# Optimization experiments

Measured on AMD Instinct MI355X. Metric: run time of the kernel, lower is better.

## Reference

```python
import jax, jax.numpy as jnp
import numpy as np


def setup_inputs() -> dict:
    key = jax.random.key(0)
    tensor = jax.random.normal(key, (1024, 32768), dtype=jnp.float32)
    return {"tensor": tensor}


def reference(tensor):
    # Fused equivalent of the per-channel Python loop: for each channel
    # (leading dim), compute min and max over all remaining elements.
    C = tensor.shape[0]
    flat = tensor.reshape(C, -1)  # [C, N]
    min_vals = jnp.min(flat, axis=1)  # [C]
    max_vals = jnp.max(flat, axis=1)  # [C]
    return min_vals, max_vals
```

## Files before the change

kernel.cpp:

```cpp
#include <hip/hip_runtime.h>
#include <math.h>


__global__ __launch_bounds__(256) void cw_minmax_kernel(
    const float* __restrict__ in, float* __restrict__ out, int nvec, int C) {
    const int c = blockIdx.x;
    const float4* __restrict__ row =
        reinterpret_cast<const float4*>(in) + (size_t)c * nvec;

    float vmin = INFINITY;
    float vmax = -INFINITY;

    for (int i = threadIdx.x; i < nvec; i += blockDim.x) {
        float4 v = row[i];
        vmin = fminf(vmin, fminf(fminf(v.x, v.y), fminf(v.z, v.w)));
        vmax = fmaxf(vmax, fmaxf(fmaxf(v.x, v.y), fmaxf(v.z, v.w)));
    }

    #pragma unroll
    for (int off = 32; off > 0; off >>= 1) {
        vmin = fminf(vmin, __shfl_down(vmin, off, 64));
        vmax = fmaxf(vmax, __shfl_down(vmax, off, 64));
    }

    __shared__ float smin[4];
    __shared__ float smax[4];
    const int wave = threadIdx.x >> 6;
    const int lane = threadIdx.x & 63;
    if (lane == 0) { smin[wave] = vmin; smax[wave] = vmax; }
    __syncthreads();

    if (threadIdx.x == 0) {
        float m = smin[0], M = smax[0];
        #pragma unroll
        for (int w = 1; w < 4; ++w) {
            m = fminf(m, smin[w]);
            M = fmaxf(M, smax[w]);
        }
        out[c] = m;
        out[C + c] = M;
    }
}

extern "C" void kernel_launch(void* const* d_in, const int* in_sizes, int n_in,
                              void* d_out, int out_size, void* d_ws, size_t ws_size,
                              hipStream_t stream) {
    const float* in = (const float*)d_in[0];
    float* out = (float*)d_out;

    const int C = out_size / 2;
    const int N = in_sizes[0] / C;
    const int nvec = N / 4;

    cw_minmax_kernel<<<C, 256, 0, stream>>>(in, out, nvec, C);
}
```

Measured before the change: 186.7 us.

## Use 1024-thread blocks with fully unrolled register-batched row loads

Replaces the strided loop with a templated kernel where each of 1024 threads issues all its float4 loads up front (8 per thread for N=32768), then reduces them. The aim is to raise memory-level parallelism and cut loop overhead so the bandwidth-bound scan keeps more loads in flight. A scalar generic fallback handles shapes that do not fit. The cost is higher register pressure and a larger cross-wave reduction of 16 waves per block.

Result: no change. 184.0 us (-1.5%).

```diff
diff --git a/kernel.cpp b/kernel.cpp
--- a/kernel.cpp
+++ b/kernel.cpp
@@ -2,29 +2,35 @@
 #include <math.h>
 
 
-__global__ __launch_bounds__(256) void cw_minmax_kernel(
+#define BS 1024
+
+template <int PER>
+__global__ __launch_bounds__(BS) void cw_minmax_spec(
     const float* __restrict__ in, float* __restrict__ out, int nvec, int C) {
     const int c = blockIdx.x;
     const float4* __restrict__ row =
         reinterpret_cast<const float4*>(in) + (size_t)c * nvec;
 
-    float vmin = INFINITY;
-    float vmax = -INFINITY;
+    float4 v[PER];
+    #pragma unroll
+    for (int k = 0; k < PER; ++k)
+        v[k] = row[threadIdx.x + k * BS];
 
-    for (int i = threadIdx.x; i < nvec; i += blockDim.x) {
-        float4 v = row[i];
-        vmin = fminf(vmin, fminf(fminf(v.x, v.y), fminf(v.z, v.w)));
-        vmax = fmaxf(vmax, fmaxf(fmaxf(v.x, v.y), fmaxf(v.z, v.w)));
+    float vmin = INFINITY, vmax = -INFINITY;
+    #pragma unroll
+    for (int k = 0; k < PER; ++k) {
+        vmin = fminf(vmin, fminf(fminf(v[k].x, v[k].y), fminf(v[k].z, v[k].w)));
+        vmax = fmaxf(vmax, fmaxf(fmaxf(v[k].x, v[k].y), fmaxf(v[k].z, v[k].w)));
     }
 
     #pragma unroll
     for (int off = 32; off > 0; off >>= 1) {
-        vmin = fminf(vmin, __shfl_down(vmin, off, 64));
-        vmax = fmaxf(vmax, __shfl_down(vmax, off, 64));
+        vmin = fminf(vmin, __shfl_xor(vmin, off, 64));
+        vmax = fmaxf(vmax, __shfl_xor(vmax, off, 64));
     }
 
-    __shared__ float smin[4];
-    __shared__ float smax[4];
+    __shared__ float smin[BS / 64];
+    __shared__ float smax[BS / 64];
     const int wave = threadIdx.x >> 6;
     const int lane = threadIdx.x & 63;
     if (lane == 0) { smin[wave] = vmin; smax[wave] = vmax; }
@@ -33,6 +39,39 @@
     if (threadIdx.x == 0) {
         float m = smin[0], M = smax[0];
         #pragma unroll
+        for (int w = 1; w < BS / 64; ++w) {
+            m = fminf(m, smin[w]);
+            M = fmaxf(M, smax[w]);
+        }
+        out[c] = m;
+        out[C + c] = M;
+    }
+}
+
+__global__ __launch_bounds__(256) void cw_minmax_generic(
+    const float* __restrict__ in, float* __restrict__ out, int N, int C) {
+    const int c = blockIdx.x;
+    const float* __restrict__ row = in + (size_t)c * N;
+
+    float vmin = INFINITY, vmax = -INFINITY;
+    for (int i = threadIdx.x; i < N; i += blockDim.x) {
+        float x = row[i];
+        vmin = fminf(vmin, x);
+        vmax = fmaxf(vmax, x);
+    }
+    #pragma unroll
+    for (int off = 32; off > 0; off >>= 1) {
+        vmin = fminf(vmin, __shfl_xor(vmin, off, 64));
+        vmax = fmaxf(vmax, __shfl_xor(vmax, off, 64));
+    }
+    __shared__ float smin[4];
+    __shared__ float smax[4];
+    const int wave = threadIdx.x >> 6;
+    const int lane = threadIdx.x & 63;
+    if (lane == 0) { smin[wave] = vmin; smax[wave] = vmax; }
+    __syncthreads();
+    if (threadIdx.x == 0) {
+        float m = smin[0], M = smax[0];
         for (int w = 1; w < 4; ++w) {
             m = fminf(m, smin[w]);
             M = fmaxf(M, smax[w]);
@@ -50,7 +89,16 @@
 
     const int C = out_size / 2;
     const int N = in_sizes[0] / C;
-    const int nvec = N / 4;
 
-    cw_minmax_kernel<<<C, 256, 0, stream>>>(in, out, nvec, C);
+    if (N % (4 * BS) == 0) {
+        const int nvec = N / 4;
+        const int per = nvec / BS;
+        switch (per) {
+            case 4:  cw_minmax_spec<4><<<C, BS, 0, stream>>>(in, out, nvec, C);  return;
+            case 8:  cw_minmax_spec<8><<<C, BS, 0, stream>>>(in, out, nvec, C);  return;
+            case 16: cw_minmax_spec<16><<<C, BS, 0, stream>>>(in, out, nvec, C); return;
+            default: break;
+        }
+    }
+    cw_minmax_generic<<<C, 256, 0, stream>>>(in, out, N, C);
 }
```
